# Optimization experiments

Hardware: AMD Instinct MI355X
Metric: run time of the kernel (lower is better)

## Reference

```python
import jax, jax.numpy as jnp
import numpy as np

BZ = 512      # number of graph pairs
NMAX = 128    # max nodes per graph (pad size; original uses sz.max())
D = 64        # node feature dim
EPS = 1e-3    # sinkhorn entropic regularization (from forward: 0.001)
ITERS = 500   # max_iters (reference runs the full budget, no early stop)
NEG = -1e5    # log(0) surrogate, safe in fp32


def setup_inputs() -> dict:
    key = jax.random.key(0)
    k1, k2, k3, k4 = jax.random.split(key, 4)
    x1 = jax.random.normal(k1, (BZ * NMAX, D), dtype=jnp.float32)
    x2 = jax.random.normal(k2, (BZ * NMAX, D), dtype=jnp.float32)
    # graph sizes in [64, 128] so no empty graphs
    sz1 = jax.random.randint(k3, (BZ,), 64, NMAX + 1, dtype=jnp.int32)
    sz2 = jax.random.randint(k4, (BZ,), 64, NMAX + 1, dtype=jnp.int32)
    return {"x1": x1, "x2": x2, "sz1": sz1, "sz2": sz2}


def _pack(x, sz, nmax):
    """Ragged [total,d] -> padded [bz,nmax,d] plus float mask [bz,nmax].
    Vectorized equivalent of the python packing loop in forward()."""
    off = jnp.cumsum(sz) - sz                       # exclusive prefix sum
    idx = off[:, None] + jnp.arange(nmax)[None, :]  # [bz, nmax]
    mask = jnp.arange(nmax)[None, :] < sz[:, None]
    g = x[jnp.clip(idx, 0, x.shape[0] - 1)] * mask[..., None].astype(x.dtype)
    return g, mask.astype(x.dtype)


def _pairwise_sq(s1, s2):
    """pairwise_distances(set1, set2, p=2): squared euclidean cost [bz,n1,n2]."""
    n1 = jnp.sum(s1 * s1, axis=-1)
    n2 = jnp.sum(s2 * s2, axis=-1)
    M = n1[:, :, None] + n2[:, None, :] - 2.0 * jnp.einsum('bnd,bmd->bnm', s1, s2)
    return jnp.maximum(M, 0.0)


def _sinkhorn(a, b, M, eps, iters):
    """Log-domain entropic Sinkhorn; padded rows/cols have a,b == 0 and
    receive NEG potentials so their transport mass is exp(NEG) ~ 0."""
    la = jnp.where(a > 0, jnp.log(jnp.where(a > 0, a, 1.0)), NEG)
    lb = jnp.where(b > 0, jnp.log(jnp.where(b > 0, b, 1.0)), NEG)
    logK = -M / eps                                  # [bz, n1, n2]

    def body(_, uv):
        u, v = uv
        v = lb - jax.scipy.special.logsumexp(logK + u[:, :, None], axis=1)
        u = la - jax.scipy.special.logsumexp(logK + v[:, None, :], axis=2)
        return (u, v)

    u0 = jnp.zeros_like(a)
    v0 = jnp.zeros_like(b)
    u, v = jax.lax.fori_loop(0, iters, body, (u0, v0))
    return jnp.exp(logK + u[:, :, None] + v[:, None, :])


def reference(x1, x2, sz1, sz2):
    set1, a = _pack(x1, sz1, NMAX)      # [bz, NMAX, D], [bz, NMAX]
    set2, bm = _pack(x2, sz2, NMAX)
    # b = b * a.sum(1,keepdim) / b.sum(1,keepdim)
    b = bm * a.sum(1, keepdims=True) / bm.sum(1, keepdims=True)
    M = _pairwise_sq(set1, set2)
    # original passes M.detach() to sinkhorn -> P is constant w.r.t. grads
    P = _sinkhorn(a, b, jax.lax.stop_gradient(M), EPS, ITERS)
    return jnp.sum(M * P, axis=(1, 2))  # [bz]
```

## Files before the change

kernel.cpp:

```cpp
#include <hip/hip_runtime.h>

#ifndef __has_builtin
#define __has_builtin(x) 0
#endif

typedef float v2f __attribute__((ext_vector_type(2)));

__device__ __forceinline__ float fexp2(float x) {
#if __has_builtin(__builtin_amdgcn_exp2f)
    return __builtin_amdgcn_exp2f(x);
#else
    return exp2f(x);
#endif
}
__device__ __forceinline__ float flog2(float x) {
#if __has_builtin(__builtin_amdgcn_logf)
    return __builtin_amdgcn_logf(x);
#else
    return log2f(x);
#endif
}
__device__ __forceinline__ float frcp(float x) {
#if __has_builtin(__builtin_amdgcn_rcpf)
    return __builtin_amdgcn_rcpf(x);
#else
    return 1.0f / x;
#endif
}

#define DPP_QX1  0xB1
#define DPP_QX2  0x4E
#define DPP_ROR4 0x124
#define DPP_ROR8 0x128

template<int CTRL>
__device__ __forceinline__ float dppf(float x) {
    return __int_as_float(__builtin_amdgcn_update_dpp(
        0, __float_as_int(x), CTRL, 0xF, 0xF, true));
}
__device__ __forceinline__ float swzx16(float x) {
    return __int_as_float(__builtin_amdgcn_ds_swizzle(__float_as_int(x), 0x401F));
}

#define NMAXN 128
#define DD    64
#define MAX_ITERS 500
#define KLOG  12

#define NEG2  (-144269.50408889634f)
#define LKSC  (-1442.6950408889634f)
#define OUTSC (-6.931471805599453e-4f)

#define LK(r, c) (((c) & 1) ? lk2[r][(c) >> 1].y : lk2[r][(c) >> 1].x)

struct SmemStage {
    float A[NMAXN * 33];
    float B[NMAXN * 33];
    float nA[NMAXN];
    float nB[NMAXN];
};
struct SmemSink {
    float2 plog[NMAXN * 10];
    float  ulog[NMAXN];
    float  pmul[NMAXN * 10];
    float  g[NMAXN];
};
union SmemU {
    SmemStage st;
    SmemSink  sk;
    char force[61440];
};

__global__ __launch_bounds__(512, 4)
void wasserstein_kernel(const float* __restrict__ x1, const float* __restrict__ x2,
                        const int* __restrict__ sz1, const int* __restrict__ sz2,
                        float* __restrict__ out)
{
    __shared__ SmemU  sm;
    __shared__ int    soff[16];
    __shared__ float  swred[8];

    const int b    = blockIdx.x;
    const int tid  = threadIdx.x;
    const int w    = tid >> 6;
    const int lane = tid & 63;
    const int rg   = lane >> 2;
    const int cg   = lane & 3;
    const int cb32 = (w << 2) | cg;

    int a1 = (tid < b) ? sz1[tid] : 0;
    int a2 = (tid < b) ? sz2[tid] : 0;
#pragma unroll
    for (int d = 1; d < 64; d <<= 1) {
        a1 += __shfl_xor(a1, d);
        a2 += __shfl_xor(a2, d);
    }
    if (lane == 0) { soff[w] = a1; soff[8 + w] = a2; }
    if (tid < NMAXN) { sm.st.nA[tid] = 0.f; sm.st.nB[tid] = 0.f; }
    __syncthreads();
    int off1 = 0, off2 = 0;
#pragma unroll
    for (int i = 0; i < 8; ++i) { off1 += soff[i]; off2 += soff[8 + i]; }
    const int n1 = sz1[b];
    const int n2 = sz2[b];

    v2f lk2[8][2];
#pragma unroll
    for (int r = 0; r < 8; ++r)
#pragma unroll
        for (int j = 0; j < 2; ++j) { lk2[r][j].x = 0.f; lk2[r][j].y = 0.f; }

    const int srow = tid >> 2;
    const int sq   = tid & 3;

    for (int ch = 0; ch < 2; ++ch) {
        const float* p1 = x1 + (size_t)(off1 + srow) * DD + ch * 32 + sq * 8;
        const float* p2 = x2 + (size_t)(off2 + srow) * DD + ch * 32 + sq * 8;
        const bool ok1 = srow < n1;
        const bool ok2 = srow < n2;
        float va[8], vb[8];
#pragma unroll
        for (int qq = 0; qq < 2; ++qq) {
            float4 t1 = ok1 ? ((const float4*)p1)[qq] : make_float4(0.f, 0.f, 0.f, 0.f);
            float4 t2 = ok2 ? ((const float4*)p2)[qq] : make_float4(0.f, 0.f, 0.f, 0.f);
            va[4*qq+0] = t1.x; va[4*qq+1] = t1.y; va[4*qq+2] = t1.z; va[4*qq+3] = t1.w;
            vb[4*qq+0] = t2.x; vb[4*qq+1] = t2.y; vb[4*qq+2] = t2.z; vb[4*qq+3] = t2.w;
        }
        float s1 = 0.f, s2v = 0.f;
#pragma unroll
        for (int j = 0; j < 8; ++j) {
            sm.st.A[srow * 33 + sq * 8 + j] = va[j];
            sm.st.B[srow * 33 + sq * 8 + j] = vb[j];
            s1  += va[j] * va[j];
            s2v += vb[j] * vb[j];
        }
        s1  += dppf<DPP_QX1>(s1);  s1  += dppf<DPP_QX2>(s1);
        s2v += dppf<DPP_QX1>(s2v); s2v += dppf<DPP_QX2>(s2v);
        if (sq == 0) { sm.st.nA[srow] += s1; sm.st.nB[srow] += s2v; }
        __syncthreads();
#pragma unroll 2
        for (int d = 0; d < 32; ++d) {
            float av[8];
            v2f bv2[2];
#pragma unroll
            for (int r = 0; r < 8; ++r) av[r] = sm.st.A[(rg + 16*r) * 33 + d];
            bv2[0].x = sm.st.B[(cb32     ) * 33 + d];
            bv2[0].y = sm.st.B[(cb32 + 32) * 33 + d];
            bv2[1].x = sm.st.B[(cb32 + 64) * 33 + d];
            bv2[1].y = sm.st.B[(cb32 + 96) * 33 + d];
#pragma unroll
            for (int r = 0; r < 8; ++r)
#pragma unroll
                for (int j = 0; j < 2; ++j)
                    lk2[r][j] += bv2[j] * av[r];
        }
        __syncthreads();
    }

    float lb[4];
    const float lbv = flog2((float)n1) - flog2((float)n2);
    {
        float rn1[8];
        v2f rn2[2];
#pragma unroll
        for (int r = 0; r < 8; ++r) rn1[r] = sm.st.nA[rg + 16*r];
        rn2[0].x = sm.st.nB[cb32];      rn2[0].y = sm.st.nB[cb32 + 32];
        rn2[1].x = sm.st.nB[cb32 + 64]; rn2[1].y = sm.st.nB[cb32 + 96];
#pragma unroll
        for (int r = 0; r < 8; ++r)
#pragma unroll
            for (int j = 0; j < 2; ++j) {
                v2f M2 = rn1[r] + rn2[j] - 2.f * lk2[r][j];
                lk2[r][j].x = fmaxf(M2.x, 0.f) * LKSC;
                lk2[r][j].y = fmaxf(M2.y, 0.f) * LKSC;
            }
#pragma unroll
        for (int c = 0; c < 4; ++c)
            lb[c] = (cb32 + 32*c < n2) ? lbv : NEG2;
    }
    __syncthreads();

    const int   crow   = tid >> 2;
    const int   q      = tid & 3;
    const float lacrow = (crow < n1) ? 0.f : NEG2;

    float uloc[8], v[4];
#pragma unroll
    for (int r = 0; r < 8; ++r) uloc[r] = 0.f;

    for (int k = 0; k < KLOG; ++k) {
        float mx[4], sc[4];
#pragma unroll
        for (int c = 0; c < 4; ++c) mx[c] = LK(0, c) + uloc[0];
#pragma unroll
        for (int r = 1; r < 8; ++r)
#pragma unroll
            for (int c = 0; c < 4; ++c)
                mx[c] = fmaxf(mx[c], LK(r, c) + uloc[r]);
#pragma unroll
        for (int c = 0; c < 4; ++c) mx[c] = fmaxf(mx[c], dppf<DPP_ROR4>(mx[c]));
#pragma unroll
        for (int c = 0; c < 4; ++c) mx[c] = fmaxf(mx[c], dppf<DPP_ROR8>(mx[c]));
#pragma unroll
        for (int c = 0; c < 4; ++c) mx[c] = fmaxf(mx[c], swzx16(mx[c]));
#pragma unroll
        for (int c = 0; c < 4; ++c) mx[c] = fmaxf(mx[c], __shfl_xor(mx[c], 32));
#pragma unroll
        for (int c = 0; c < 4; ++c) sc[c] = fexp2(LK(0, c) + uloc[0] - mx[c]);
#pragma unroll
        for (int r = 1; r < 8; ++r)
#pragma unroll
            for (int c = 0; c < 4; ++c)
                sc[c] += fexp2(LK(r, c) + uloc[r] - mx[c]);
#pragma unroll
        for (int c = 0; c < 4; ++c) sc[c] += dppf<DPP_ROR4>(sc[c]);
#pragma unroll
        for (int c = 0; c < 4; ++c) sc[c] += dppf<DPP_ROR8>(sc[c]);
#pragma unroll
        for (int c = 0; c < 4; ++c) sc[c] += swzx16(sc[c]);
#pragma unroll
        for (int c = 0; c < 4; ++c) sc[c] += __shfl_xor(sc[c], 32);
#pragma unroll
        for (int c = 0; c < 4; ++c)
            v[c] = lb[c] - (mx[c] + flog2(sc[c]));

#pragma unroll
        for (int r = 0; r < 8; ++r) {
            float mr = LK(r, 0) + v[0];
#pragma unroll
            for (int c = 1; c < 4; ++c) mr = fmaxf(mr, LK(r, c) + v[c]);
            mr = fmaxf(mr, dppf<DPP_QX1>(mr));
            mr = fmaxf(mr, dppf<DPP_QX2>(mr));
            float sr = fexp2(LK(r, 0) + v[0] - mr);
#pragma unroll
            for (int c = 1; c < 4; ++c) sr += fexp2(LK(r, c) + v[c] - mr);
            sr += dppf<DPP_QX1>(sr);
            sr += dppf<DPP_QX2>(sr);
            if ((r & 3) == cg)
                sm.sk.plog[(rg + 16*r) * 10 + w] = make_float2(mr, sr);
        }
        __syncthreads();

        {
            float4 t = *(const float4*)&sm.sk.plog[crow * 10 + 2 * q];
            float m = fmaxf(t.x, t.z);
            float s = t.y * fexp2(t.x - m) + t.w * fexp2(t.z - m);
            float mo = dppf<DPP_QX1>(m), so = dppf<DPP_QX1>(s);
            float mm = fmaxf(m, mo);
            s = s * fexp2(m - mm) + so * fexp2(mo - mm); m = mm;
            mo = dppf<DPP_QX2>(m); so = dppf<DPP_QX2>(s);
            mm = fmaxf(m, mo);
            s = s * fexp2(m - mm) + so * fexp2(mo - mm); m = mm;
            if (q == 0) sm.sk.ulog[crow] = lacrow - (m + flog2(s));
        }
        __syncthreads();

#pragma unroll
        for (int r = 0; r < 8; ++r) uloc[r] = sm.sk.ulog[rg + 16*r];
    }

    v2f Q2[8][2];
#pragma unroll
    for (int r = 0; r < 8; ++r)
#pragma unroll
        for (int j = 0; j < 2; ++j) {
            Q2[r][j].x = fexp2(LK(r, 2*j    ) + uloc[r] + v[2*j    ]);
            Q2[r][j].y = fexp2(LK(r, 2*j + 1) + uloc[r] + v[2*j + 1]);
        }

    const float bmulv = (float)n1 / (float)n2;
    float fm[4];
#pragma unroll
    for (int c = 0; c < 4; ++c)
        fm[c] = (cb32 + 32*c < n2) ? bmulv : 0.f;
    const float gmask = (crow < n1) ? 1.f : 0.f;

    float gl[8];
#pragma unroll
    for (int r = 0; r < 8; ++r) gl[r] = 1.f;

    for (int k = KLOG; k < MAX_ITERS; ++k) {
        v2f p0 = Q2[0][0] * gl[0];
        v2f p1 = Q2[1][0] * gl[1];
        v2f q0 = Q2[0][1] * gl[0];
        v2f q1 = Q2[1][1] * gl[1];
#pragma unroll
        for (int r = 2; r < 8; r += 2) {
            p0 += Q2[r  ][0] * gl[r  ];
            p1 += Q2[r+1][0] * gl[r+1];
            q0 += Q2[r  ][1] * gl[r  ];
            q1 += Q2[r+1][1] * gl[r+1];
        }
        v2f s20 = p0 + p1;
        v2f s21 = q0 + q1;
        float s[4] = { s20.x, s20.y, s21.x, s21.y };
#pragma unroll
        for (int c = 0; c < 4; ++c) s[c] += dppf<DPP_ROR4>(s[c]);
#pragma unroll
        for (int c = 0; c < 4; ++c) s[c] += dppf<DPP_ROR8>(s[c]);
#pragma unroll
        for (int c = 0; c < 4; ++c) s[c] += swzx16(s[c]);
#pragma unroll
        for (int c = 0; c < 4; ++c) s[c] += __shfl_xor(s[c], 32);
        v2f f2[2];
        f2[0].x = fm[0] * frcp(fmaxf(s[0], 1e-37f));
        f2[0].y = fm[1] * frcp(fmaxf(s[1], 1e-37f));
        f2[1].x = fm[2] * frcp(fmaxf(s[2], 1e-37f));
        f2[1].y = fm[3] * frcp(fmaxf(s[3], 1e-37f));

#pragma unroll
        for (int r = 0; r < 8; ++r) {
            Q2[r][0] *= f2[0];
            Q2[r][1] *= f2[1];
            v2f tt = Q2[r][0] + Q2[r][1];
            float t = tt.x + tt.y;
            t += dppf<DPP_QX1>(t);
            t += dppf<DPP_QX2>(t);
            if ((r & 3) == cg)
                sm.sk.pmul[(rg + 16*r) * 10 + w] = t;
        }
        __syncthreads();

        {
            float2 t2 = *(const float2*)&sm.sk.pmul[crow * 10 + 2 * q];
            float t = t2.x + t2.y;
            t += dppf<DPP_QX1>(t);
            t += dppf<DPP_QX2>(t);
            float gg = gmask * frcp(fmaxf(t, 1e-37f));
            if (q == 0) sm.sk.g[crow] = gg;
        }
        __syncthreads();

#pragma unroll
        for (int r = 0; r < 8; ++r) gl[r] = sm.sk.g[rg + 16*r];

        if ((k & 15) == 15) {
#pragma unroll
            for (int r = 0; r < 8; ++r) {
                Q2[r][0] *= gl[r];
                Q2[r][1] *= gl[r];
                gl[r] = 1.f;
            }
        }
    }

    v2f acc2; acc2.x = 0.f; acc2.y = 0.f;
#pragma unroll
    for (int r = 0; r < 8; ++r)
#pragma unroll
        for (int j = 0; j < 2; ++j)
            acc2 += lk2[r][j] * (Q2[r][j] * gl[r]);
    float acc = acc2.x + acc2.y;
    acc += dppf<DPP_QX1>(acc);
    acc += dppf<DPP_QX2>(acc);
    acc += dppf<DPP_ROR4>(acc);
    acc += dppf<DPP_ROR8>(acc);
    acc += swzx16(acc);
    acc += __shfl_xor(acc, 32);
    if (lane == 0) swred[w] = acc;
    __syncthreads();
    if (tid == 0) {
        float s = 0.f;
#pragma unroll
        for (int i = 0; i < 8; ++i) s += swred[i];
        out[b] = s * OUTSC;
    }
}

extern "C" void kernel_launch(void* const* d_in, const int* in_sizes, int n_in,
                              void* d_out, int out_size, void* d_ws, size_t ws_size,
                              hipStream_t stream) {
    const float* x1  = (const float*)d_in[0];
    const float* x2  = (const float*)d_in[1];
    const int*   sz1 = (const int*)d_in[2];
    const int*   sz2 = (const int*)d_in[3];
    float* out = (float*)d_out;
    hipLaunchKernelGGL(wasserstein_kernel, dim3(512), dim3(512), 0, stream,
                       x1, x2, sz1, sz2, out);
}
```

Baseline: 660.7 us.

## Split each pair across 1024 threads with 16 matrix cells per thread

Doubles the block size from 512 to 1024 threads, so each thread holds an 8x2 tile of the cost/transport matrix instead of 8x4. Shared-memory partial buffers grow to 16 wave columns, and the row reductions gain an extra DPP stage across 8 lanes. The aim is more parallelism per graph pair and lower register pressure, hiding latency in the 500-iteration Sinkhorn loop. In exchange, each iteration's barriers and cross-wave shared-memory reductions now synchronise 16 waves instead of 8, and with 512 blocks the per-CU occupancy may change.

```diff
diff --git a/kernel.cpp b/kernel.cpp
--- a/kernel.cpp
+++ b/kernel.cpp
@@ -32,6 +32,7 @@
 #define DPP_QX2  0x4E
 #define DPP_ROR4 0x124
 #define DPP_ROR8 0x128
+#define DPP_RHM  0x141
 
 template<int CTRL>
 __device__ __forceinline__ float dppf(float x) {
@@ -50,8 +51,6 @@
 #define NEG2  (-144269.50408889634f)
 #define LKSC  (-1442.6950408889634f)
 #define OUTSC (-6.931471805599453e-4f)
-
-#define LK(r, c) (((c) & 1) ? lk2[r][(c) >> 1].y : lk2[r][(c) >> 1].x)
 
 struct SmemStage {
     float A[NMAXN * 33];
@@ -60,33 +59,37 @@
     float nB[NMAXN];
 };
 struct SmemSink {
-    float2 plog[NMAXN * 10];
-    float  ulog[NMAXN];
-    float  pmul[NMAXN * 10];
-    float  g[NMAXN];
+    float pm[NMAXN * 17];
+    float ps[NMAXN * 17];
+    float pmul[NMAXN * 17];
+    float ug[NMAXN];
 };
 union SmemU {
     SmemStage st;
     SmemSink  sk;
-    char force[61440];
 };
 
-__global__ __launch_bounds__(512, 4)
+__global__ __launch_bounds__(1024, 8)
 void wasserstein_kernel(const float* __restrict__ x1, const float* __restrict__ x2,
                         const int* __restrict__ sz1, const int* __restrict__ sz2,
                         float* __restrict__ out)
 {
     __shared__ SmemU  sm;
-    __shared__ int    soff[16];
-    __shared__ float  swred[8];
+    __shared__ int    soff[32];
+    __shared__ float  swred[16];
 
     const int b    = blockIdx.x;
     const int tid  = threadIdx.x;
     const int w    = tid >> 6;
     const int lane = tid & 63;
-    const int rg   = lane >> 2;
+    const int rg   = lane >> 4;
+    (void)rg;
+    const int rg4  = lane >> 2;
     const int cg   = lane & 3;
-    const int cb32 = (w << 2) | cg;
+    const int cw   = (w << 2) | cg;
+
+    const int crow = tid >> 3;
+    const int q8   = tid & 7;
 
     int a1 = (tid < b) ? sz1[tid] : 0;
     int a2 = (tid < b) ? sz2[tid] : 0;
@@ -95,184 +98,160 @@
         a1 += __shfl_xor(a1, d);
         a2 += __shfl_xor(a2, d);
     }
-    if (lane == 0) { soff[w] = a1; soff[8 + w] = a2; }
+    if (lane == 0) { soff[w] = a1; soff[16 + w] = a2; }
     if (tid < NMAXN) { sm.st.nA[tid] = 0.f; sm.st.nB[tid] = 0.f; }
     __syncthreads();
     int off1 = 0, off2 = 0;
 #pragma unroll
-    for (int i = 0; i < 8; ++i) { off1 += soff[i]; off2 += soff[8 + i]; }
+    for (int i = 0; i < 16; ++i) { off1 += soff[i]; off2 += soff[16 + i]; }
     const int n1 = sz1[b];
     const int n2 = sz2[b];
 
-    v2f lk2[8][2];
-#pragma unroll
-    for (int r = 0; r < 8; ++r)
-#pragma unroll
-        for (int j = 0; j < 2; ++j) { lk2[r][j].x = 0.f; lk2[r][j].y = 0.f; }
-
-    const int srow = tid >> 2;
-    const int sq   = tid & 3;
+    v2f lk2[8];
+#pragma unroll
+    for (int r = 0; r < 8; ++r) { lk2[r].x = 0.f; lk2[r].y = 0.f; }
+
+    const int srow = tid >> 3;
+    const int sq   = tid & 7;
 
     for (int ch = 0; ch < 2; ++ch) {
-        const float* p1 = x1 + (size_t)(off1 + srow) * DD + ch * 32 + sq * 8;
-        const float* p2 = x2 + (size_t)(off2 + srow) * DD + ch * 32 + sq * 8;
+        const float* p1 = x1 + (size_t)(off1 + srow) * DD + ch * 32 + sq * 4;
+        const float* p2 = x2 + (size_t)(off2 + srow) * DD + ch * 32 + sq * 4;
         const bool ok1 = srow < n1;
         const bool ok2 = srow < n2;
-        float va[8], vb[8];
-#pragma unroll
-        for (int qq = 0; qq < 2; ++qq) {
-            float4 t1 = ok1 ? ((const float4*)p1)[qq] : make_float4(0.f, 0.f, 0.f, 0.f);
-            float4 t2 = ok2 ? ((const float4*)p2)[qq] : make_float4(0.f, 0.f, 0.f, 0.f);
-            va[4*qq+0] = t1.x; va[4*qq+1] = t1.y; va[4*qq+2] = t1.z; va[4*qq+3] = t1.w;
-            vb[4*qq+0] = t2.x; vb[4*qq+1] = t2.y; vb[4*qq+2] = t2.z; vb[4*qq+3] = t2.w;
-        }
+        float4 t1 = ok1 ? *(const float4*)p1 : make_float4(0.f, 0.f, 0.f, 0.f);
+        float4 t2 = ok2 ? *(const float4*)p2 : make_float4(0.f, 0.f, 0.f, 0.f);
+        float va[4] = { t1.x, t1.y, t1.z, t1.w };
+        float vb[4] = { t2.x, t2.y, t2.z, t2.w };
         float s1 = 0.f, s2v = 0.f;
 #pragma unroll
-        for (int j = 0; j < 8; ++j) {
-            sm.st.A[srow * 33 + sq * 8 + j] = va[j];
-            sm.st.B[srow * 33 + sq * 8 + j] = vb[j];
+        for (int j = 0; j < 4; ++j) {
+            sm.st.A[srow * 33 + sq * 4 + j] = va[j];
+            sm.st.B[srow * 33 + sq * 4 + j] = vb[j];
             s1  += va[j] * va[j];
             s2v += vb[j] * vb[j];
         }
-        s1  += dppf<DPP_QX1>(s1);  s1  += dppf<DPP_QX2>(s1);
-        s2v += dppf<DPP_QX1>(s2v); s2v += dppf<DPP_QX2>(s2v);
+        s1  += dppf<DPP_QX1>(s1);  s1  += dppf<DPP_QX2>(s1);  s1  += dppf<DPP_RHM>(s1);
+        s2v += dppf<DPP_QX1>(s2v); s2v += dppf<DPP_QX2>(s2v); s2v += dppf<DPP_RHM>(s2v);
         if (sq == 0) { sm.st.nA[srow] += s1; sm.st.nB[srow] += s2v; }
         __syncthreads();
 #pragma unroll 2
         for (int d = 0; d < 32; ++d) {
             float av[8];
-            v2f bv2[2];
-#pragma unroll
-            for (int r = 0; r < 8; ++r) av[r] = sm.st.A[(rg + 16*r) * 33 + d];
-            bv2[0].x = sm.st.B[(cb32     ) * 33 + d];
-            bv2[0].y = sm.st.B[(cb32 + 32) * 33 + d];
-            bv2[1].x = sm.st.B[(cb32 + 64) * 33 + d];
-            bv2[1].y = sm.st.B[(cb32 + 96) * 33 + d];
+#pragma unroll
+            for (int r = 0; r < 8; ++r) av[r] = sm.st.A[(rg4 + 16*r) * 33 + d];
+            v2f bv2;
+            bv2.x = sm.st.B[(cw     ) * 33 + d];
+            bv2.y = sm.st.B[(cw + 64) * 33 + d];
 #pragma unroll
             for (int r = 0; r < 8; ++r)
-#pragma unroll
-                for (int j = 0; j < 2; ++j)
-                    lk2[r][j] += bv2[j] * av[r];
-        }
-        __syncthreads();
-    }
-
-    float lb[4];
+                lk2[r] += bv2 * av[r];
+        }
+        __syncthreads();
+    }
+
+    v2f lb2;
     const float lbv = flog2((float)n1) - flog2((float)n2);
     {
-        float rn1[8];
-        v2f rn2[2];
-#pragma unroll
-        for (int r = 0; r < 8; ++r) rn1[r] = sm.st.nA[rg + 16*r];
-        rn2[0].x = sm.st.nB[cb32];      rn2[0].y = sm.st.nB[cb32 + 32];
-        rn2[1].x = sm.st.nB[cb32 + 64]; rn2[1].y = sm.st.nB[cb32 + 96];
-#pragma unroll
-        for (int r = 0; r < 8; ++r)
-#pragma unroll
-            for (int j = 0; j < 2; ++j) {
-                v2f M2 = rn1[r] + rn2[j] - 2.f * lk2[r][j];
-                lk2[r][j].x = fmaxf(M2.x, 0.f) * LKSC;
-                lk2[r][j].y = fmaxf(M2.y, 0.f) * LKSC;
-            }
-#pragma unroll
-        for (int c = 0; c < 4; ++c)
-            lb[c] = (cb32 + 32*c < n2) ? lbv : NEG2;
+        v2f rn2;
+        rn2.x = sm.st.nB[cw];
+        rn2.y = sm.st.nB[cw + 64];
+#pragma unroll
+        for (int r = 0; r < 8; ++r) {
+            float rn1 = sm.st.nA[rg4 + 16*r];
+            v2f M2 = rn1 + rn2 - 2.f * lk2[r];
+            lk2[r].x = fmaxf(M2.x, 0.f) * LKSC;
+            lk2[r].y = fmaxf(M2.y, 0.f) * LKSC;
+        }
+        lb2.x = (cw      < n2) ? lbv : NEG2;
+        lb2.y = (cw + 64 < n2) ? lbv : NEG2;
     }
     __syncthreads();
 
-    const int   crow   = tid >> 2;
-    const int   q      = tid & 3;
     const float lacrow = (crow < n1) ? 0.f : NEG2;
 
-    float uloc[8], v[4];
+    float uloc[8];
+    v2f vv;
 #pragma unroll
     for (int r = 0; r < 8; ++r) uloc[r] = 0.f;
 
     for (int k = 0; k < KLOG; ++k) {
-        float mx[4], sc[4];
-#pragma unroll
-        for (int c = 0; c < 4; ++c) mx[c] = LK(0, c) + uloc[0];
-#pragma unroll
-        for (int r = 1; r < 8; ++r)
-#pragma unroll
-            for (int c = 0; c < 4; ++c)
-                mx[c] = fmaxf(mx[c], LK(r, c) + uloc[r]);
-#pragma unroll
-        for (int c = 0; c < 4; ++c) mx[c] = fmaxf(mx[c], dppf<DPP_ROR4>(mx[c]));
-#pragma unroll
-        for (int c = 0; c < 4; ++c) mx[c] = fmaxf(mx[c], dppf<DPP_ROR8>(mx[c]));
-#pragma unroll
-        for (int c = 0; c < 4; ++c) mx[c] = fmaxf(mx[c], swzx16(mx[c]));
-#pragma unroll
-        for (int c = 0; c < 4; ++c) mx[c] = fmaxf(mx[c], __shfl_xor(mx[c], 32));
-#pragma unroll
-        for (int c = 0; c < 4; ++c) sc[c] = fexp2(LK(0, c) + uloc[0] - mx[c]);
-#pragma unroll
-        for (int r = 1; r < 8; ++r)
-#pragma unroll
-            for (int c = 0; c < 4; ++c)
-                sc[c] += fexp2(LK(r, c) + uloc[r] - mx[c]);
-#pragma unroll
-        for (int c = 0; c < 4; ++c) sc[c] += dppf<DPP_ROR4>(sc[c]);
-#pragma unroll
-        for (int c = 0; c < 4; ++c) sc[c] += dppf<DPP_ROR8>(sc[c]);
-#pragma unroll
-        for (int c = 0; c < 4; ++c) sc[c] += swzx16(sc[c]);
-#pragma unroll
-        for (int c = 0; c < 4; ++c) sc[c] += __shfl_xor(sc[c], 32);
-#pragma unroll
-        for (int c = 0; c < 4; ++c)
-            v[c] = lb[c] - (mx[c] + flog2(sc[c]));
+        float mx0 = lk2[0].x + uloc[0];
+        float mx1 = lk2[0].y + uloc[0];
+#pragma unroll
+        for (int r = 1; r < 8; ++r) {
+            mx0 = fmaxf(mx0, lk2[r].x + uloc[r]);
+            mx1 = fmaxf(mx1, lk2[r].y + uloc[r]);
+        }
+        mx0 = fmaxf(mx0, dppf<DPP_ROR4>(mx0)); mx1 = fmaxf(mx1, dppf<DPP_ROR4>(mx1));
+        mx0 = fmaxf(mx0, dppf<DPP_ROR8>(mx0)); mx1 = fmaxf(mx1, dppf<DPP_ROR8>(mx1));
+        mx0 = fmaxf(mx0, swzx16(mx0));         mx1 = fmaxf(mx1, swzx16(mx1));
+        mx0 = fmaxf(mx0, __shfl_xor(mx0, 32)); mx1 = fmaxf(mx1, __shfl_xor(mx1, 32));
+
+        float sc0 = fexp2(lk2[0].x + uloc[0] - mx0);
+        float sc1 = fexp2(lk2[0].y + uloc[0] - mx1);
+#pragma unroll
+        for (int r = 1; r < 8; ++r) {
+            sc0 += fexp2(lk2[r].x + uloc[r] - mx0);
+            sc1 += fexp2(lk2[r].y + uloc[r] - mx1);
+        }
+        sc0 += dppf<DPP_ROR4>(sc0); sc1 += dppf<DPP_ROR4>(sc1);
+        sc0 += dppf<DPP_ROR8>(sc0); sc1 += dppf<DPP_ROR8>(sc1);
+        sc0 += swzx16(sc0);         sc1 += swzx16(sc1);
+        sc0 += __shfl_xor(sc0, 32); sc1 += __shfl_xor(sc1, 32);
+
+        vv.x = lb2.x - (mx0 + flog2(sc0));
+        vv.y = lb2.y - (mx1 + flog2(sc1));
 
 #pragma unroll
         for (int r = 0; r < 8; ++r) {
-            float mr = LK(r, 0) + v[0];
-#pragma unroll
-            for (int c = 1; c < 4; ++c) mr = fmaxf(mr, LK(r, c) + v[c]);
+            float mr = fmaxf(lk2[r].x + vv.x, lk2[r].y + vv.y);
             mr = fmaxf(mr, dppf<DPP_QX1>(mr));
             mr = fmaxf(mr, dppf<DPP_QX2>(mr));
-            float sr = fexp2(LK(r, 0) + v[0] - mr);
-#pragma unroll
-            for (int c = 1; c < 4; ++c) sr += fexp2(LK(r, c) + v[c] - mr);
+            float sr = fexp2(lk2[r].x + vv.x - mr) + fexp2(lk2[r].y + vv.y - mr);
             sr += dppf<DPP_QX1>(sr);
             sr += dppf<DPP_QX2>(sr);
-            if ((r & 3) == cg)
-                sm.sk.plog[(rg + 16*r) * 10 + w] = make_float2(mr, sr);
+            if ((r & 3) == cg) {
+                const int row = rg4 + 16*r;
+                sm.sk.pm[row * 17 + w] = mr;
+                sm.sk.ps[row * 17 + w] = sr;
+            }
         }
         __syncthreads();
 
         {
-            float4 t = *(const float4*)&sm.sk.plog[crow * 10 + 2 * q];
-            float m = fmaxf(t.x, t.z);
-            float s = t.y * fexp2(t.x - m) + t.w * fexp2(t.z - m);
+            float m0 = sm.sk.pm[crow * 17 + 2*q8], m1 = sm.sk.pm[crow * 17 + 2*q8 + 1];
+            float s0 = sm.sk.ps[crow * 17 + 2*q8], s1 = sm.sk.ps[crow * 17 + 2*q8 + 1];
+            float m = fmaxf(m0, m1);
+            float s = s0 * fexp2(m0 - m) + s1 * fexp2(m1 - m);
             float mo = dppf<DPP_QX1>(m), so = dppf<DPP_QX1>(s);
             float mm = fmaxf(m, mo);
             s = s * fexp2(m - mm) + so * fexp2(mo - mm); m = mm;
             mo = dppf<DPP_QX2>(m); so = dppf<DPP_QX2>(s);
             mm = fmaxf(m, mo);
             s = s * fexp2(m - mm) + so * fexp2(mo - mm); m = mm;
-            if (q == 0) sm.sk.ulog[crow] = lacrow - (m + flog2(s));
-        }
-        __syncthreads();
-
-#pragma unroll
-        for (int r = 0; r < 8; ++r) uloc[r] = sm.sk.ulog[rg + 16*r];
-    }
-
-    v2f Q2[8][2];
-#pragma unroll
-    for (int r = 0; r < 8; ++r)
-#pragma unroll
-        for (int j = 0; j < 2; ++j) {
-            Q2[r][j].x = fexp2(LK(r, 2*j    ) + uloc[r] + v[2*j    ]);
-            Q2[r][j].y = fexp2(LK(r, 2*j + 1) + uloc[r] + v[2*j + 1]);
-        }
+            mo = dppf<DPP_RHM>(m); so = dppf<DPP_RHM>(s);
+            mm = fmaxf(m, mo);
+            s = s * fexp2(m - mm) + so * fexp2(mo - mm); m = mm;
+            if (q8 == 0) sm.sk.ug[crow] = lacrow - (m + flog2(s));
+        }
+        __syncthreads();
+
+#pragma unroll
+        for (int r = 0; r < 8; ++r) uloc[r] = sm.sk.ug[rg4 + 16*r];
+    }
+
+    v2f Q2[8];
+#pragma unroll
+    for (int r = 0; r < 8; ++r) {
+        Q2[r].x = fexp2(lk2[r].x + uloc[r] + vv.x);
+        Q2[r].y = fexp2(lk2[r].y + uloc[r] + vv.y);
+    }
 
     const float bmulv = (float)n1 / (float)n2;
-    float fm[4];
-#pragma unroll
-    for (int c = 0; c < 4; ++c)
-        fm[c] = (cb32 + 32*c < n2) ? bmulv : 0.f;
+    v2f fm2;
+    fm2.x = (cw      < n2) ? bmulv : 0.f;
+    fm2.y = (cw + 64 < n2) ? bmulv : 0.f;
     const float gmask = (crow < n1) ? 1.f : 0.f;
 
     float gl[8];
@@ -280,65 +259,53 @@
     for (int r = 0; r < 8; ++r) gl[r] = 1.f;
 
     for (int k = KLOG; k < MAX_ITERS; ++k) {
-        v2f p0 = Q2[0][0] * gl[0];
-        v2f p1 = Q2[1][0] * gl[1];
-        v2f q0 = Q2[0][1] * gl[0];
-        v2f q1 = Q2[1][1] * gl[1];
+        v2f p0 = Q2[0] * gl[0];
+        v2f p1 = Q2[1] * gl[1];
 #pragma unroll
         for (int r = 2; r < 8; r += 2) {
-            p0 += Q2[r  ][0] * gl[r  ];
-            p1 += Q2[r+1][0] * gl[r+1];
-            q0 += Q2[r  ][1] * gl[r  ];
-            q1 += Q2[r+1][1] * gl[r+1];
-        }
-        v2f s20 = p0 + p1;
-        v2f s21 = q0 + q1;
-        float s[4] = { s20.x, s20.y, s21.x, s21.y };
-#pragma unroll
-        for (int c = 0; c < 4; ++c) s[c] += dppf<DPP_ROR4>(s[c]);
-#pragma unroll
-        for (int c = 0; c < 4; ++c) s[c] += dppf<DPP_ROR8>(s[c]);
-#pragma unroll
-        for (int c = 0; c < 4; ++c) s[c] += swzx16(s[c]);
-#pragma unroll
-        for (int c = 0; c < 4; ++c) s[c] += __shfl_xor(s[c], 32);
-        v2f f2[2];
-        f2[0].x = fm[0] * frcp(fmaxf(s[0], 1e-37f));
-        f2[0].y = fm[1] * frcp(fmaxf(s[1], 1e-37f));
-        f2[1].x = fm[2] * frcp(fmaxf(s[2], 1e-37f));
-        f2[1].y = fm[3] * frcp(fmaxf(s[3], 1e-37f));
+            p0 += Q2[r  ] * gl[r  ];
+            p1 += Q2[r+1] * gl[r+1];
+        }
+        v2f s2 = p0 + p1;
+        float s0 = s2.x, s1 = s2.y;
+        s0 += dppf<DPP_ROR4>(s0); s1 += dppf<DPP_ROR4>(s1);
+        s0 += dppf<DPP_ROR8>(s0); s1 += dppf<DPP_ROR8>(s1);
+        s0 += swzx16(s0);         s1 += swzx16(s1);
+        s0 += __shfl_xor(s0, 32); s1 += __shfl_xor(s1, 32);
+        v2f f2;
+        f2.x = fm2.x * frcp(fmaxf(s0, 1e-37f));
+        f2.y = fm2.y * frcp(fmaxf(s1, 1e-37f));
 
 #pragma unroll
         for (int r = 0; r < 8; ++r) {
-            Q2[r][0] *= f2[0];
-            Q2[r][1] *= f2[1];
-            v2f tt = Q2[r][0] + Q2[r][1];
-            float t = tt.x + tt.y;
+            Q2[r] *= f2;
+            float t = Q2[r].x + Q2[r].y;
             t += dppf<DPP_QX1>(t);
             t += dppf<DPP_QX2>(t);
             if ((r & 3) == cg)
-                sm.sk.pmul[(rg + 16*r) * 10 + w] = t;
+                sm.sk.pmul[(rg4 + 16*r) * 17 + w] = t;
         }
         __syncthreads();
 
         {
-            float2 t2 = *(const float2*)&sm.sk.pmul[crow * 10 + 2 * q];
-            float t = t2.x + t2.y;
+            float t0 = sm.sk.pmul[crow * 17 + 2*q8];
+            float t1 = sm.sk.pmul[crow * 17 + 2*q8 + 1];
+            float t = t0 + t1;
             t += dppf<DPP_QX1>(t);
             t += dppf<DPP_QX2>(t);
+            t += dppf<DPP_RHM>(t);
             float gg = gmask * frcp(fmaxf(t, 1e-37f));
-            if (q == 0) sm.sk.g[crow] = gg;
-        }
-        __syncthreads();
-
-#pragma unroll
-        for (int r = 0; r < 8; ++r) gl[r] = sm.sk.g[rg + 16*r];
+            if (q8 == 0) sm.sk.ug[crow] = gg;
+        }
+        __syncthreads();
+
+#pragma unroll
+        for (int r = 0; r < 8; ++r) gl[r] = sm.sk.ug[rg4 + 16*r];
 
         if ((k & 15) == 15) {
 #pragma unroll
             for (int r = 0; r < 8; ++r) {
-                Q2[r][0] *= gl[r];
-                Q2[r][1] *= gl[r];
+                Q2[r] *= gl[r];
                 gl[r] = 1.f;
             }
         }
@@ -347,9 +314,7 @@
     v2f acc2; acc2.x = 0.f; acc2.y = 0.f;
 #pragma unroll
     for (int r = 0; r < 8; ++r)
-#pragma unroll
-        for (int j = 0; j < 2; ++j)
-            acc2 += lk2[r][j] * (Q2[r][j] * gl[r]);
+        acc2 += lk2[r] * (Q2[r] * gl[r]);
     float acc = acc2.x + acc2.y;
     acc += dppf<DPP_QX1>(acc);
     acc += dppf<DPP_QX2>(acc);
@@ -362,7 +327,7 @@
     if (tid == 0) {
         float s = 0.f;
 #pragma unroll
-        for (int i = 0; i < 8; ++i) s += swred[i];
+        for (int i = 0; i < 16; ++i) s += swred[i];
         out[b] = s * OUTSC;
     }
 }
@@ -375,6 +340,6 @@
     const int*   sz1 = (const int*)d_in[2];
     const int*   sz2 = (const int*)d_in[3];
     float* out = (float*)d_out;
-    hipLaunchKernelGGL(wasserstein_kernel, dim3(512), dim3(512), 0, stream,
+    hipLaunchKernelGGL(wasserstein_kernel, dim3(512), dim3(1024), 0, stream,
                        x1, x2, sz1, sz2, out);
 }
```

New measurement: 765.1 us. 15.8% more time.

## Specialize Sinkhorn scaling loop on active row count and defer column-factor application

Applied to the files above, without the earlier changes.

Moves the multiplicative Sinkhorn loop into a template specialized on the number of 16-row groups that hold valid rows (4..8), chosen at runtime from n1. Rows past the graph size are skipped, so smaller graphs do less arithmetic per iteration. The column factor is no longer multiplied into Q every iteration; it is folded into the row-sum product and applied only at the periodic renormalisation and in the final accumulation. The cost is five instantiated copies of the loop, which adds code size and could change register allocation.

```diff
diff --git a/kernel.cpp b/kernel.cpp
--- a/kernel.cpp
+++ b/kernel.cpp
@@ -71,6 +71,98 @@
     char force[61440];
 };
 
+template<int NR>
+__device__ __forceinline__ float sink_mul(
+    v2f (&lk2)[8][2], const float (&uloc)[8], const float (&v)[4],
+    const float (&fm)[4], float gmask,
+    SmemU& sm, int rg, int cg, int w, int crow, int q)
+{
+    v2f Q2[NR][2];
+#pragma unroll
+    for (int r = 0; r < NR; ++r)
+#pragma unroll
+        for (int j = 0; j < 2; ++j) {
+            Q2[r][j].x = fexp2(LK(r, 2*j    ) + uloc[r] + v[2*j    ]);
+            Q2[r][j].y = fexp2(LK(r, 2*j + 1) + uloc[r] + v[2*j + 1]);
+        }
+    float gl[NR];
+#pragma unroll
+    for (int r = 0; r < NR; ++r) gl[r] = 1.f;
+    v2f fc2[2];
+    fc2[0].x = fc2[0].y = 0.f;
+    fc2[1] = fc2[0];
+
+    for (int k = KLOG; k < MAX_ITERS; ++k) {
+        v2f p0 = Q2[0][0] * gl[0];
+        v2f q0 = Q2[0][1] * gl[0];
+        v2f p1; p1.x = 0.f; p1.y = 0.f;
+        v2f q1 = p1;
+        if constexpr (NR > 1) { p1 = Q2[1][0] * gl[1]; q1 = Q2[1][1] * gl[1]; }
+#pragma unroll
+        for (int r = 2; r < NR; ++r) {
+            if ((r & 1) == 0) { p0 += Q2[r][0] * gl[r]; q0 += Q2[r][1] * gl[r]; }
+            else              { p1 += Q2[r][0] * gl[r]; q1 += Q2[r][1] * gl[r]; }
+        }
+        v2f s20 = p0 + p1;
+        v2f s21 = q0 + q1;
+        float s[4] = { s20.x, s20.y, s21.x, s21.y };
+#pragma unroll
+        for (int c = 0; c < 4; ++c) s[c] += dppf<DPP_ROR4>(s[c]);
+#pragma unroll
+        for (int c = 0; c < 4; ++c) s[c] += dppf<DPP_ROR8>(s[c]);
+#pragma unroll
+        for (int c = 0; c < 4; ++c) s[c] += swzx16(s[c]);
+#pragma unroll
+        for (int c = 0; c < 4; ++c) s[c] += __shfl_xor(s[c], 32);
+        fc2[0].x = fm[0] * frcp(fmaxf(s[0], 1e-37f));
+        fc2[0].y = fm[1] * frcp(fmaxf(s[1], 1e-37f));
+        fc2[1].x = fm[2] * frcp(fmaxf(s[2], 1e-37f));
+        fc2[1].y = fm[3] * frcp(fmaxf(s[3], 1e-37f));
+
+#pragma unroll
+        for (int r = 0; r < NR; ++r) {
+            v2f t2 = Q2[r][0] * fc2[0];
+            t2 += Q2[r][1] * fc2[1];
+            float t = t2.x + t2.y;
+            t += dppf<DPP_QX1>(t);
+            t += dppf<DPP_QX2>(t);
+            if ((r & 3) == cg)
+                sm.sk.pmul[(rg + 16*r) * 10 + w] = t;
+        }
+        __syncthreads();
+
+        {
+            float2 t2r = *(const float2*)&sm.sk.pmul[crow * 10 + 2 * q];
+            float t = t2r.x + t2r.y;
+            t += dppf<DPP_QX1>(t);
+            t += dppf<DPP_QX2>(t);
+            float gg = gmask * frcp(fmaxf(t, 1e-37f));
+            if (q == 0) sm.sk.g[crow] = gg;
+        }
+        __syncthreads();
+
+#pragma unroll
+        for (int r = 0; r < NR; ++r) gl[r] = sm.sk.g[rg + 16*r];
+
+        if ((k & 15) == 15) {
+#pragma unroll
+            for (int r = 0; r < NR; ++r) {
+                Q2[r][0] *= fc2[0] * gl[r];
+                Q2[r][1] *= fc2[1] * gl[r];
+                gl[r] = 1.f;
+            }
+        }
+    }
+
+    v2f acc2; acc2.x = 0.f; acc2.y = 0.f;
+#pragma unroll
+    for (int r = 0; r < NR; ++r)
+#pragma unroll
+        for (int j = 0; j < 2; ++j)
+            acc2 += lk2[r][j] * (Q2[r][j] * (fc2[j] * gl[r]));
+    return acc2.x + acc2.y;
+}
+
 __global__ __launch_bounds__(512, 4)
 void wasserstein_kernel(const float* __restrict__ x1, const float* __restrict__ x2,
                         const int* __restrict__ sz1, const int* __restrict__ sz2,
@@ -259,15 +351,6 @@
         for (int r = 0; r < 8; ++r) uloc[r] = sm.sk.ulog[rg + 16*r];
     }
 
-    v2f Q2[8][2];
-#pragma unroll
-    for (int r = 0; r < 8; ++r)
-#pragma unroll
-        for (int j = 0; j < 2; ++j) {
-            Q2[r][j].x = fexp2(LK(r, 2*j    ) + uloc[r] + v[2*j    ]);
-            Q2[r][j].y = fexp2(LK(r, 2*j + 1) + uloc[r] + v[2*j + 1]);
-        }
-
     const float bmulv = (float)n1 / (float)n2;
     float fm[4];
 #pragma unroll
@@ -275,82 +358,16 @@
         fm[c] = (cb32 + 32*c < n2) ? bmulv : 0.f;
     const float gmask = (crow < n1) ? 1.f : 0.f;
 
-    float gl[8];
-#pragma unroll
-    for (int r = 0; r < 8; ++r) gl[r] = 1.f;
-
-    for (int k = KLOG; k < MAX_ITERS; ++k) {
-        v2f p0 = Q2[0][0] * gl[0];
-        v2f p1 = Q2[1][0] * gl[1];
-        v2f q0 = Q2[0][1] * gl[0];
-        v2f q1 = Q2[1][1] * gl[1];
-#pragma unroll
-        for (int r = 2; r < 8; r += 2) {
-            p0 += Q2[r  ][0] * gl[r  ];
-            p1 += Q2[r+1][0] * gl[r+1];
-            q0 += Q2[r  ][1] * gl[r  ];
-            q1 += Q2[r+1][1] * gl[r+1];
-        }
-        v2f s20 = p0 + p1;
-        v2f s21 = q0 + q1;
-        float s[4] = { s20.x, s20.y, s21.x, s21.y };
-#pragma unroll
-        for (int c = 0; c < 4; ++c) s[c] += dppf<DPP_ROR4>(s[c]);
-#pragma unroll
-        for (int c = 0; c < 4; ++c) s[c] += dppf<DPP_ROR8>(s[c]);
-#pragma unroll
-        for (int c = 0; c < 4; ++c) s[c] += swzx16(s[c]);
-#pragma unroll
-        for (int c = 0; c < 4; ++c) s[c] += __shfl_xor(s[c], 32);
-        v2f f2[2];
-        f2[0].x = fm[0] * frcp(fmaxf(s[0], 1e-37f));
-        f2[0].y = fm[1] * frcp(fmaxf(s[1], 1e-37f));
-        f2[1].x = fm[2] * frcp(fmaxf(s[2], 1e-37f));
-        f2[1].y = fm[3] * frcp(fmaxf(s[3], 1e-37f));
-
-#pragma unroll
-        for (int r = 0; r < 8; ++r) {
-            Q2[r][0] *= f2[0];
-            Q2[r][1] *= f2[1];
-            v2f tt = Q2[r][0] + Q2[r][1];
-            float t = tt.x + tt.y;
-            t += dppf<DPP_QX1>(t);
-            t += dppf<DPP_QX2>(t);
-            if ((r & 3) == cg)
-                sm.sk.pmul[(rg + 16*r) * 10 + w] = t;
-        }
-        __syncthreads();
-
-        {
-            float2 t2 = *(const float2*)&sm.sk.pmul[crow * 10 + 2 * q];
-            float t = t2.x + t2.y;
-            t += dppf<DPP_QX1>(t);
-            t += dppf<DPP_QX2>(t);
-            float gg = gmask * frcp(fmaxf(t, 1e-37f));
-            if (q == 0) sm.sk.g[crow] = gg;
-        }
-        __syncthreads();
-
-#pragma unroll
-        for (int r = 0; r < 8; ++r) gl[r] = sm.sk.g[rg + 16*r];
-
-        if ((k & 15) == 15) {
-#pragma unroll
-            for (int r = 0; r < 8; ++r) {
-                Q2[r][0] *= gl[r];
-                Q2[r][1] *= gl[r];
-                gl[r] = 1.f;
-            }
-        }
-    }
-
-    v2f acc2; acc2.x = 0.f; acc2.y = 0.f;
-#pragma unroll
-    for (int r = 0; r < 8; ++r)
-#pragma unroll
-        for (int j = 0; j < 2; ++j)
-            acc2 += lk2[r][j] * (Q2[r][j] * gl[r]);
-    float acc = acc2.x + acc2.y;
+    float acc;
+    const int nr = (n1 + 15) >> 4;
+    switch (nr) {
+        case 4:  acc = sink_mul<4>(lk2, uloc, v, fm, gmask, sm, rg, cg, w, crow, q); break;
+        case 5:  acc = sink_mul<5>(lk2, uloc, v, fm, gmask, sm, rg, cg, w, crow, q); break;
+        case 6:  acc = sink_mul<6>(lk2, uloc, v, fm, gmask, sm, rg, cg, w, crow, q); break;
+        case 7:  acc = sink_mul<7>(lk2, uloc, v, fm, gmask, sm, rg, cg, w, crow, q); break;
+        default: acc = sink_mul<8>(lk2, uloc, v, fm, gmask, sm, rg, cg, w, crow, q); break;
+    }
+
     acc += dppf<DPP_QX1>(acc);
     acc += dppf<DPP_QX2>(acc);
     acc += dppf<DPP_ROR4>(acc);
```

Result: faster. 639.2 us (-3.3%).
